# Kernel optimization log

Measured on AMD Instinct MI355X. Metric: run time of the kernel, lower is better.

Reference implementation:

```python
import jax, jax.numpy as jnp
import numpy as np

DICT_SIZE = 16384
D_MODEL = 1024
TOP_K = 8
B, T = 2, 2048


def setup_inputs() -> dict:
    key = jax.random.key(0)
    k1, k2, k3 = jax.random.split(key, 3)
    x = jax.random.normal(k1, (B, T, D_MODEL), dtype=jnp.float32)
    # nn.Linear weight, scaled small like the torch init style
    W_enc = jax.random.normal(k2, (DICT_SIZE, D_MODEL), dtype=jnp.float32) * 0.02
    # unified dictionary: randn * 0.02 per UnifiedDictionaryCore
    W_dict = jax.random.normal(k3, (DICT_SIZE, D_MODEL), dtype=jnp.float32) * 0.02
    return {"x": x, "W_enc": W_enc, "W_dict": W_dict}


def reference(x, W_enc, W_dict):
    # encoder: Linear(d_model -> dict_size), no bias
    coeffs = jnp.einsum("btd,md->btm", x, W_enc)  # [B,T,dict_size]
    topk_vals, topk_idx = jax.lax.top_k(coeffs, TOP_K)  # [B,T,K]
    # scatter-into-zeros then dense matmul == weighted sum of gathered dict rows
    # (top-k indices are unique per token, so the math is identical)
    rows = W_dict[topk_idx]  # [B,T,K,d_model]
    offset = jnp.einsum("btk,btkd->btd", topk_vals, rows)
    # sparse_coeffs.abs().mean() over the full dense [B,T,dict_size] tensor;
    # only the top-k entries are nonzero
    sparsity_loss = jnp.sum(jnp.abs(topk_vals)) / (coeffs.size)
    return offset, sparsity_loss
```

## Files before the change

kernel.cpp:

```cpp
#include <hip/hip_runtime.h>
#include <float.h>
#include <stdint.h>

constexpr int D_MODEL = 1024;
constexpr int DICT    = 16384;
constexpr int TOPK    = 8;
constexpr int NCAND   = 16;
constexpr int NTOK    = 4096;
constexpr int NTILE   = 128;
constexpr long long COEFF_COUNT = (long long)NTOK * DICT;

typedef __attribute__((ext_vector_type(8))) __bf16 bf16x8;
typedef __attribute__((ext_vector_type(4))) float  floatx4;

__device__ __forceinline__ unsigned short f2bf(float f) {
    unsigned int u = __float_as_uint(f);
    u = u + 0x7fffu + ((u >> 16) & 1u);
    return (unsigned short)(u >> 16);
}

__device__ __forceinline__ void async16(void* lds, const void* g) {
    __builtin_amdgcn_global_load_lds(
        (__attribute__((address_space(1))) void*)g,
        (__attribute__((address_space(3))) void*)lds, 16, 0, 0);
}

__global__ __launch_bounds__(256) void ssod_cvt2(const float4* __restrict__ xs, ushort4* __restrict__ xd, int nx4,
                                                 const float4* __restrict__ ws, ushort4* __restrict__ wd, int nw4) {
    const int i = blockIdx.x * 256 + threadIdx.x;
    if (i < nx4) {
        const float4 v = xs[i];
        ushort4 o; o.x = f2bf(v.x); o.y = f2bf(v.y); o.z = f2bf(v.z); o.w = f2bf(v.w);
        xd[i] = o;
    } else {
        const int j = i - nx4;
        if (j < nw4) {
            const float4 v = ws[j];
            ushort4 o; o.x = f2bf(v.x); o.y = f2bf(v.y); o.z = f2bf(v.z); o.w = f2bf(v.w);
            wd[j] = o;
        }
    }
}

constexpr size_t R1OFF = (size_t)128 * (D_MODEL * 2);

#define STAGE_A(buf_, t_) do {                                               \
    const char* s_ = pA + (size_t)(t_) * 64;                                 \
    char* d_ = (char*)&As[(buf_)][0] + wave * 1024;                          \
    async16(d_, s_); async16(d_ + 8192, s_ + R1OFF);                         \
} while (0)

#define STAGE_B(buf_, t_) do {                                               \
    const char* s_ = pB + (size_t)(t_) * 64;                                 \
    char* d_ = (char*)&Bs[(buf_)][0] + wave * 1024;                          \
    async16(d_, s_); async16(d_ + 8192, s_ + R1OFF);                         \
} while (0)

#define MFMA4(a_, r_)                                                                        \
    acc[r_][0] = __builtin_amdgcn_mfma_f32_16x16x32_bf16(a_, bq0, acc[r_][0], 0, 0, 0);      \
    acc[r_][1] = __builtin_amdgcn_mfma_f32_16x16x32_bf16(a_, bq1, acc[r_][1], 0, 0, 0);      \
    acc[r_][2] = __builtin_amdgcn_mfma_f32_16x16x32_bf16(a_, bq2, acc[r_][2], 0, 0, 0);      \
    acc[r_][3] = __builtin_amdgcn_mfma_f32_16x16x32_bf16(a_, bq3, acc[r_][3], 0, 0, 0);

#define TILE_BODY(T_, DOSTAGE_)                                              \
  {                                                                          \
    const int buf_ = (T_) & 3;                                               \
    const char* ab_ = (const char*)As + buf_ * 16384 + aob;                  \
    const char* bb_ = (const char*)Bs + buf_ * 16384 + bob;                  \
    bf16x8 af0 = *(const bf16x8*)(ab_);                                      \
    bf16x8 af1 = *(const bf16x8*)(ab_ + 1024);                               \
    bf16x8 af2 = *(const bf16x8*)(ab_ + 2048);                               \
    bf16x8 af3 = *(const bf16x8*)(ab_ + 3072);                               \
    bf16x8 bq0 = *(const bf16x8*)(bb_);                                      \
    bf16x8 bq1 = *(const bf16x8*)(bb_ + 1024);                               \
    bf16x8 bq2 = *(const bf16x8*)(bb_ + 2048);                               \
    bf16x8 bq3 = *(const bf16x8*)(bb_ + 3072);                               \
    if (DOSTAGE_) { STAGE_A(((T_) + 3) & 3, (T_) + 3); }                     \
    __builtin_amdgcn_s_barrier();                                            \
    asm volatile("s_waitcnt lgkmcnt(0)" ::: "memory");                       \
    __builtin_amdgcn_s_setprio(1);                                           \
    MFMA4(af0, 0); MFMA4(af1, 1); MFMA4(af2, 2); MFMA4(af3, 3);              \
    __builtin_amdgcn_s_setprio(0);                                           \
    __builtin_amdgcn_s_barrier();                                            \
    bf16x8 ag0 = *(const bf16x8*)(ab_ + 4096);                               \
    bf16x8 ag1 = *(const bf16x8*)(ab_ + 5120);                               \
    bf16x8 ag2 = *(const bf16x8*)(ab_ + 6144);                               \
    bf16x8 ag3 = *(const bf16x8*)(ab_ + 7168);                               \
    if (DOSTAGE_) { STAGE_B(((T_) + 3) & 3, (T_) + 3); }                     \
    __builtin_amdgcn_s_barrier();                                            \
    asm volatile("s_waitcnt lgkmcnt(0)" ::: "memory");                       \
    __builtin_amdgcn_s_setprio(1);                                           \
    MFMA4(ag0, 4); MFMA4(ag1, 5); MFMA4(ag2, 6); MFMA4(ag3, 7);              \
    __builtin_amdgcn_s_setprio(0);                                           \
  }

#define TILE_CLOSE(VMI)                                                      \
    asm volatile("s_waitcnt vmcnt(" #VMI ")" ::: "memory");                  \
    __builtin_amdgcn_s_barrier();

__global__ __launch_bounds__(512, 2) void ssod_gemm_bf16(const unsigned short* __restrict__ A,
                                                         const unsigned short* __restrict__ B,
                                                         unsigned short* __restrict__ C,
                                                         unsigned short* __restrict__ tmax,
                                                         int mtiles) {
    __shared__ __align__(16) unsigned short As[4][8192];
    __shared__ __align__(16) unsigned short Bs[4][8192];

    const int tid  = threadIdx.x;
    const int wave = tid >> 6;
    const int lane = tid & 63;

    const int nwg = mtiles * 64;
    const int cpx = nwg >> 3;
    const int bid = blockIdx.x;
    const int vid = (bid & 7) * cpx + (bid >> 3);
    const int bn  = vid & 63;
    const int bm  = vid >> 6;

    const int wm = wave >> 2;
    const int wn = wave & 3;
    const int fr = lane & 15;
    const int kg = lane >> 4;

    const int sR   = tid >> 3;
    const int sinp = ((tid & 7) * 16) ^ ((sR & 7) << 4);
    const int smr  = 2 * sR + (sinp >> 6);
    const int skb  = sinp & 63;
    const char* pA = (const char*)(A + (size_t)bm * 256 * D_MODEL) + (size_t)smr * (D_MODEL * 2) + skb;
    const char* pB = (const char*)(B + (size_t)bn * 256 * D_MODEL) + (size_t)smr * (D_MODEL * 2) + skb;

    const int swz = ((((fr & 1) << 6) | (kg << 4)) ^ (((fr >> 1) & 7) << 4));
    const int aob = (wm * 64 + (fr >> 1)) * 128 + swz;
    const int bob = (wn * 32 + (fr >> 1)) * 128 + swz;

    floatx4 acc[8][4];
    #pragma unroll
    for (int i = 0; i < 8; ++i)
        #pragma unroll
        for (int j = 0; j < 4; ++j) acc[i][j] = floatx4{0.f, 0.f, 0.f, 0.f};

    STAGE_A(0, 0); STAGE_B(0, 0);
    STAGE_A(1, 1); STAGE_B(1, 1);
    STAGE_A(2, 2); STAGE_B(2, 2);
    TILE_CLOSE(8)

    #pragma unroll 1
    for (int T = 0; T < 29; ++T) {
        TILE_BODY(T, true)
        TILE_CLOSE(8)
    }
    TILE_BODY(29, false)
    TILE_CLOSE(4)
    TILE_BODY(30, false)
    TILE_CLOSE(0)
    TILE_BODY(31, false)

    __syncthreads();
    unsigned int* rmax = (unsigned int*)&As[0][0];
    rmax[tid] = 0;
    __syncthreads();

    const int col  = lane & 15;
    const int rq   = lane >> 4;
    const int half = wn >> 1;
    const size_t colbase = (size_t)bn * 256 + wn * 64 + col;

    #pragma unroll
    for (int mf = 0; mf < 8; ++mf) {
        const int rowl = wm * 128 + mf * 16 + rq * 4;
        unsigned int rm[4] = {0, 0, 0, 0};
        #pragma unroll
        for (int nf = 0; nf < 4; ++nf) {
            unsigned short* cp = C + (size_t)(bm * 256 + rowl) * DICT + colbase + nf * 16;
            #pragma unroll
            for (int r = 0; r < 4; ++r) {
                const unsigned short bfv = f2bf(acc[mf][nf][r]);
                cp[(size_t)r * DICT] = bfv;
                rm[r] = max(rm[r], (unsigned int)(bfv ^ 0x8000u));
            }
        }
        #pragma unroll
        for (int r = 0; r < 4; ++r) {
            unsigned int m = rm[r];
            m = max(m, (unsigned int)__shfl_xor((int)m, 1, 64));
            m = max(m, (unsigned int)__shfl_xor((int)m, 2, 64));
            m = max(m, (unsigned int)__shfl_xor((int)m, 4, 64));
            m = max(m, (unsigned int)__shfl_xor((int)m, 8, 64));
            if (col == 0) atomicMax(&rmax[(rowl + r) * 2 + half], m);
        }
    }
    __syncthreads();
    {
        const int row = tid >> 1;
        tmax[(size_t)(bm * 256 + row) * NTILE + bn * 2 + (tid & 1)] = (unsigned short)rmax[tid];
    }
}

#undef TILE_BODY
#undef TILE_CLOSE
#undef MFMA4
#undef STAGE_A
#undef STAGE_B

__device__ __forceinline__ bool tk_better(float v1, int i1, float v2, int i2) {
    return (v1 > v2) || (v1 == v2 && i1 < i2);
}

__global__ __launch_bounds__(256) void ssod_select_refine(const unsigned short* __restrict__ coeffs,
                                                          const unsigned short* __restrict__ tmax,
                                                          const float* __restrict__ x,
                                                          const float* __restrict__ Wenc,
                                                          const float* __restrict__ Wdict,
                                                          float* __restrict__ outp,
                                                          float* __restrict__ tsum,
                                                          int tokBase) {
    const int tl   = blockIdx.x;
    const int t    = tokBase + tl;
    const int tid  = threadIdx.x;
    const int lane = tid & 63;
    const int wave = tid >> 6;

    __shared__ unsigned int keys[128];
    __shared__ int   tlist[64];
    __shared__ int   ncnt, kcnt;
    __shared__ unsigned int sTau;
    __shared__ float xs[D_MODEL];
    __shared__ int   cidx[NCAND];
    __shared__ float cval[NCAND];
    __shared__ float sval[TOPK];
    __shared__ int   sidx[TOPK];

    ((float4*)xs)[tid] = ((const float4*)(x + (size_t)t * D_MODEL))[tid];
    if (tid == 0) { ncnt = 0; kcnt = 0; }
    __syncthreads();

    const unsigned short* tmrow = tmax + (size_t)t * NTILE;
    if (wave == 0) {
        const unsigned int u = ((const unsigned int*)tmrow)[lane];
        unsigned int v0 = u & 0xFFFFu, v1 = u >> 16;
        for (int k = 2; k <= 128; k <<= 1) {
            for (int j = k >> 1; j >= 1; j >>= 1) {
                if (j == 64) {
                    const unsigned int a = max(v0, v1), b = min(v0, v1);
                    v0 = a; v1 = b;
                } else {
                    const unsigned int p0 = __shfl_xor(v0, j, 64);
                    const unsigned int p1 = __shfl_xor(v1, j, 64);
                    const bool tm0 = ((lane & j) == 0) ^ ((( lane      ) & k) != 0);
                    const bool tm1 = ((lane & j) == 0) ^ (((lane + 64) & k) != 0);
                    v0 = tm0 ? max(v0, p0) : min(v0, p0);
                    v1 = tm1 ? max(v1, p1) : min(v1, p1);
                }
            }
        }
        if (lane == 15) sTau = v0;
    }
    __syncthreads();
    const unsigned int tau = sTau;

    if (tid < NTILE) {
        if ((unsigned int)tmrow[tid] >= tau) {
            const int p = atomicAdd(&ncnt, 1);
            if (p < 64) tlist[p] = tid;
        }
    }
    __syncthreads();
    const int nq = min(ncnt, 64);

    const uint4* row4 = (const uint4*)(coeffs + (size_t)tl * DICT);
    for (int j = tid; j < nq * 16; j += 256) {
        const int tile = tlist[j >> 4];
        const int sub  = j & 15;
        const uint4 p = row4[tile * 16 + sub];
        unsigned int w[4] = {p.x ^ 0x80008000u, p.y ^ 0x80008000u,
                             p.z ^ 0x80008000u, p.w ^ 0x80008000u};
        const int base = tile * 128 + sub * 8;
        #pragma unroll
        for (int h = 0; h < 4; ++h) {
            const unsigned int lo = w[h] & 0xFFFFu, hi = w[h] >> 16;
            if (lo >= tau) {
                const int q = atomicAdd(&kcnt, 1);
                if (q < 128) keys[q] = (lo << 16) | (unsigned)(16383 - (base + h * 2));
            }
            if (hi >= tau) {
                const int q = atomicAdd(&kcnt, 1);
                if (q < 128) keys[q] = (hi << 16) | (unsigned)(16383 - (base + h * 2 + 1));
            }
        }
    }
    __syncthreads();
    const int m = min(kcnt, 128);
    for (int i = m + tid; i < 128; i += 256) keys[i] = 0;
    __syncthreads();

    if (wave == 0) {
        unsigned int v0 = keys[lane], v1 = keys[lane + 64];
        for (int k = 2; k <= 128; k <<= 1) {
            for (int j = k >> 1; j >= 1; j >>= 1) {
                if (j == 64) {
                    const unsigned int a = max(v0, v1), b = min(v0, v1);
                    v0 = a; v1 = b;
                } else {
                    const unsigned int p0 = __shfl_xor(v0, j, 64);
                    const unsigned int p1 = __shfl_xor(v1, j, 64);
                    const bool tm0 = ((lane & j) == 0) ^ ((( lane      ) & k) != 0);
                    const bool tm1 = ((lane & j) == 0) ^ (((lane + 64) & k) != 0);
                    v0 = tm0 ? max(v0, p0) : min(v0, p0);
                    v1 = tm1 ? max(v1, p1) : min(v1, p1);
                }
            }
        }
        if (lane < NCAND) cidx[lane] = 16383 - (int)(v0 & 0xFFFFu);
    }
    __syncthreads();

    const float4* xs4 = (const float4*)xs;
    float4 xv[4];
    #pragma unroll
    for (int q = 0; q < 4; ++q) xv[q] = xs4[q * 64 + lane];

    float4 wv[4][4];
    #pragma unroll
    for (int s = 0; s < 4; ++s) {
        const float4* wr4 = (const float4*)(Wenc + (size_t)cidx[s * 4 + wave] * D_MODEL);
        #pragma unroll
        for (int q = 0; q < 4; ++q) wv[s][q] = wr4[q * 64 + lane];
    }
    #pragma unroll
    for (int s = 0; s < 4; ++s) {
        float sum = 0.f;
        #pragma unroll
        for (int q = 0; q < 4; ++q)
            sum += xv[q].x * wv[s][q].x + xv[q].y * wv[s][q].y +
                   xv[q].z * wv[s][q].z + xv[q].w * wv[s][q].w;
        #pragma unroll
        for (int off = 32; off > 0; off >>= 1) sum += __shfl_down(sum, off, 64);
        if (lane == 0) cval[s * 4 + wave] = sum;
    }
    __syncthreads();

    if (tid < NCAND) {
        const float v = cval[tid];
        const int  ix = cidx[tid];
        int rank = 0;
        #pragma unroll
        for (int j = 0; j < NCAND; ++j)
            rank += (j != tid) && tk_better(cval[j], cidx[j], v, ix);
        if (rank < TOPK) { sval[rank] = v; sidx[rank] = ix; }
    }
    __syncthreads();
    if (tid == 0) {
        float s = 0.f;
        #pragma unroll
        for (int k = 0; k < TOPK; ++k) s += fabsf(sval[k]);
        tsum[t] = s;
    }

    const int dd = tid * 4;
    float4 a = make_float4(0.f, 0.f, 0.f, 0.f);
    #pragma unroll
    for (int k = 0; k < TOPK; ++k) {
        const float4 r = *(const float4*)(Wdict + (size_t)sidx[k] * D_MODEL + dd);
        const float s = sval[k];
        a.x += s * r.x; a.y += s * r.y; a.z += s * r.z; a.w += s * r.w;
    }
    *(float4*)(outp + (size_t)t * D_MODEL + dd) = a;
}

__global__ __launch_bounds__(256) void ssod_loss(const float* __restrict__ tsum,
                                                 float* __restrict__ out) {
    float s = 0.f;
    for (int i = threadIdx.x; i < NTOK; i += 256) s += tsum[i];
    #pragma unroll
    for (int off = 32; off > 0; off >>= 1) s += __shfl_down(s, off, 64);
    __shared__ float wsum[4];
    if ((threadIdx.x & 63) == 0) wsum[threadIdx.x >> 6] = s;
    __syncthreads();
    if (threadIdx.x == 0) {
        const float tot = wsum[0] + wsum[1] + wsum[2] + wsum[3];
        out[(size_t)NTOK * D_MODEL] = tot / (float)COEFF_COUNT;
    }
}

extern "C" void kernel_launch(void* const* d_in, const int* in_sizes, int n_in,
                              void* d_out, int out_size, void* d_ws, size_t ws_size,
                              hipStream_t stream) {
    const float* x     = (const float*)d_in[0];
    const float* Wenc  = (const float*)d_in[1];
    const float* Wdict = (const float*)d_in[2];
    float* out = (float*)d_out;

    char* ws = (char*)d_ws;
    size_t off = 0;
    unsigned short* xbf  = (unsigned short*)(ws + off); off += (size_t)NTOK * D_MODEL * 2;
    unsigned short* wbf  = (unsigned short*)(ws + off); off += (size_t)DICT * D_MODEL * 2;
    unsigned short* tmax = (unsigned short*)(ws + off); off += (size_t)NTOK * NTILE * 2;
    float* tsum = (float*)(ws + off);                   off += (size_t)NTOK * 4;
    unsigned short* coeffs = (unsigned short*)(ws + off);

    const size_t remain = (ws_size > off) ? (ws_size - off) : 0;
    int chunk = 512;
    if (remain >= (size_t)4096 * DICT * 2) chunk = 4096;
    else if (remain >= (size_t)2048 * DICT * 2) chunk = 2048;
    else if (remain >= (size_t)1024 * DICT * 2) chunk = 1024;

    const int nx4 = NTOK * D_MODEL / 4;
    const int nw4 = DICT * D_MODEL / 4;
    ssod_cvt2<<<(nx4 + nw4 + 255) / 256, 256, 0, stream>>>(
        (const float4*)x, (ushort4*)xbf, nx4, (const float4*)Wenc, (ushort4*)wbf, nw4);

    for (int tokBase = 0; tokBase < NTOK; tokBase += chunk) {
        const int mtiles = chunk / 256;
        ssod_gemm_bf16<<<mtiles * 64, 512, 0, stream>>>(xbf + (size_t)tokBase * D_MODEL, wbf, coeffs,
                                                        tmax + (size_t)tokBase * NTILE, mtiles);
        ssod_select_refine<<<chunk, 256, 0, stream>>>(coeffs, tmax, x, Wenc, Wdict, out, tsum, tokBase);
    }
    ssod_loss<<<1, 256, 0, stream>>>(tsum, out);
}
```

Baseline: 397.6 us.

## Double-buffer GEMM register fragments and swap MFMA operands for packed coefficient stores

The bf16 GEMM main loop now keeps two register sets of LDS fragments and prefetches the next tile's fragments between the two halves of the current tile's MFMAs. This replaces the old split-barrier scheme and cuts the barriers per tile from three to one. The MFMA operands are swapped so each lane holds four consecutive dictionary columns, which lets the epilogue write 8-byte packed stores instead of scalar 2-byte strided stores. The row-max reduction needs fewer shuffles as a result. The workgroup-to-tile mapping is also simplified to a fixed 8x8 swizzle, which raises register pressure at occupancy 2 and may change L2 locality.

```diff
diff --git a/kernel.cpp b/kernel.cpp
--- a/kernel.cpp
+++ b/kernel.cpp
@@ -56,53 +56,50 @@
     async16(d_, s_); async16(d_ + 8192, s_ + R1OFF);                         \
 } while (0)
 
-#define MFMA4(a_, r_)                                                                        \
-    acc[r_][0] = __builtin_amdgcn_mfma_f32_16x16x32_bf16(a_, bq0, acc[r_][0], 0, 0, 0);      \
-    acc[r_][1] = __builtin_amdgcn_mfma_f32_16x16x32_bf16(a_, bq1, acc[r_][1], 0, 0, 0);      \
-    acc[r_][2] = __builtin_amdgcn_mfma_f32_16x16x32_bf16(a_, bq2, acc[r_][2], 0, 0, 0);      \
-    acc[r_][3] = __builtin_amdgcn_mfma_f32_16x16x32_bf16(a_, bq3, acc[r_][3], 0, 0, 0);
-
-#define TILE_BODY(T_, DOSTAGE_)                                              \
-  {                                                                          \
-    const int buf_ = (T_) & 3;                                               \
-    const char* ab_ = (const char*)As + buf_ * 16384 + aob;                  \
-    const char* bb_ = (const char*)Bs + buf_ * 16384 + bob;                  \
-    bf16x8 af0 = *(const bf16x8*)(ab_);                                      \
-    bf16x8 af1 = *(const bf16x8*)(ab_ + 1024);                               \
-    bf16x8 af2 = *(const bf16x8*)(ab_ + 2048);                               \
-    bf16x8 af3 = *(const bf16x8*)(ab_ + 3072);                               \
-    bf16x8 bq0 = *(const bf16x8*)(bb_);                                      \
-    bf16x8 bq1 = *(const bf16x8*)(bb_ + 1024);                               \
-    bf16x8 bq2 = *(const bf16x8*)(bb_ + 2048);                               \
-    bf16x8 bq3 = *(const bf16x8*)(bb_ + 3072);                               \
-    if (DOSTAGE_) { STAGE_A(((T_) + 3) & 3, (T_) + 3); }                     \
-    __builtin_amdgcn_s_barrier();                                            \
-    asm volatile("s_waitcnt lgkmcnt(0)" ::: "memory");                       \
+#define LOADFRAGS(P, buf_) do {                                              \
+    const char* ab_ = (const char*)As + (buf_) * 16384 + aob;                \
+    const char* bb_ = (const char*)Bs + (buf_) * 16384 + bob;                \
+    P##af0 = *(const bf16x8*)(ab_);                                          \
+    P##af1 = *(const bf16x8*)(ab_ + 1024);                                   \
+    P##af2 = *(const bf16x8*)(ab_ + 2048);                                   \
+    P##af3 = *(const bf16x8*)(ab_ + 3072);                                   \
+    P##af4 = *(const bf16x8*)(ab_ + 4096);                                   \
+    P##af5 = *(const bf16x8*)(ab_ + 5120);                                   \
+    P##af6 = *(const bf16x8*)(ab_ + 6144);                                   \
+    P##af7 = *(const bf16x8*)(ab_ + 7168);                                   \
+    P##bq0 = *(const bf16x8*)(bb_);                                          \
+    P##bq1 = *(const bf16x8*)(bb_ + 1024);                                   \
+    P##bq2 = *(const bf16x8*)(bb_ + 2048);                                   \
+    P##bq3 = *(const bf16x8*)(bb_ + 3072);                                   \
+} while (0)
+
+#define MROW(P, AF, m_)                                                                     \
+    acc[m_][0] = __builtin_amdgcn_mfma_f32_16x16x32_bf16(P##bq0, AF, acc[m_][0], 0, 0, 0);  \
+    acc[m_][1] = __builtin_amdgcn_mfma_f32_16x16x32_bf16(P##bq1, AF, acc[m_][1], 0, 0, 0);  \
+    acc[m_][2] = __builtin_amdgcn_mfma_f32_16x16x32_bf16(P##bq2, AF, acc[m_][2], 0, 0, 0);  \
+    acc[m_][3] = __builtin_amdgcn_mfma_f32_16x16x32_bf16(P##bq3, AF, acc[m_][3], 0, 0, 0);
+
+#define C1(P) MROW(P, P##af0, 0) MROW(P, P##af1, 1) MROW(P, P##af2, 2) MROW(P, P##af3, 3)
+#define C2(P) MROW(P, P##af4, 4) MROW(P, P##af5, 5) MROW(P, P##af6, 6) MROW(P, P##af7, 7)
+
+#define TILE(T_, CONS, LOAD, DOSTAGE, VMI) do {                              \
+    if (DOSTAGE) {                                                           \
+        STAGE_A(((T_) + 3) & 3, (T_) + 3);                                   \
+        STAGE_B(((T_) + 3) & 3, (T_) + 3);                                   \
+    }                                                                        \
+    asm volatile("s_waitcnt vmcnt(" #VMI ")" ::: "memory");                  \
+    asm volatile("s_barrier" ::: "memory");                                  \
     __builtin_amdgcn_s_setprio(1);                                           \
-    MFMA4(af0, 0); MFMA4(af1, 1); MFMA4(af2, 2); MFMA4(af3, 3);              \
+    C1(CONS)                                                                 \
+    LOADFRAGS(LOAD, ((T_) + 1) & 3);                                         \
+    C2(CONS)                                                                 \
     __builtin_amdgcn_s_setprio(0);                                           \
-    __builtin_amdgcn_s_barrier();                                            \
-    bf16x8 ag0 = *(const bf16x8*)(ab_ + 4096);                               \
-    bf16x8 ag1 = *(const bf16x8*)(ab_ + 5120);                               \
-    bf16x8 ag2 = *(const bf16x8*)(ab_ + 6144);                               \
-    bf16x8 ag3 = *(const bf16x8*)(ab_ + 7168);                               \
-    if (DOSTAGE_) { STAGE_B(((T_) + 3) & 3, (T_) + 3); }                     \
-    __builtin_amdgcn_s_barrier();                                            \
-    asm volatile("s_waitcnt lgkmcnt(0)" ::: "memory");                       \
-    __builtin_amdgcn_s_setprio(1);                                           \
-    MFMA4(ag0, 4); MFMA4(ag1, 5); MFMA4(ag2, 6); MFMA4(ag3, 7);              \
-    __builtin_amdgcn_s_setprio(0);                                           \
-  }
-
-#define TILE_CLOSE(VMI)                                                      \
-    asm volatile("s_waitcnt vmcnt(" #VMI ")" ::: "memory");                  \
-    __builtin_amdgcn_s_barrier();
+} while (0)
 
 __global__ __launch_bounds__(512, 2) void ssod_gemm_bf16(const unsigned short* __restrict__ A,
                                                          const unsigned short* __restrict__ B,
                                                          unsigned short* __restrict__ C,
-                                                         unsigned short* __restrict__ tmax,
-                                                         int mtiles) {
+                                                         unsigned short* __restrict__ tmax) {
     __shared__ __align__(16) unsigned short As[4][8192];
     __shared__ __align__(16) unsigned short Bs[4][8192];
 
@@ -110,12 +107,9 @@
     const int wave = tid >> 6;
     const int lane = tid & 63;
 
-    const int nwg = mtiles * 64;
-    const int cpx = nwg >> 3;
     const int bid = blockIdx.x;
-    const int vid = (bid & 7) * cpx + (bid >> 3);
-    const int bn  = vid & 63;
-    const int bm  = vid >> 6;
+    const int bn  = (bid & 7) * 8 + ((bid >> 3) & 7);
+    const int bm  = bid >> 6;
 
     const int wm = wave >> 2;
     const int wn = wave & 3;
@@ -139,66 +133,69 @@
         #pragma unroll
         for (int j = 0; j < 4; ++j) acc[i][j] = floatx4{0.f, 0.f, 0.f, 0.f};
 
+    bf16x8 RA_af0, RA_af1, RA_af2, RA_af3, RA_af4, RA_af5, RA_af6, RA_af7;
+    bf16x8 RA_bq0, RA_bq1, RA_bq2, RA_bq3;
+    bf16x8 RB_af0, RB_af1, RB_af2, RB_af3, RB_af4, RB_af5, RB_af6, RB_af7;
+    bf16x8 RB_bq0, RB_bq1, RB_bq2, RB_bq3;
+
     STAGE_A(0, 0); STAGE_B(0, 0);
     STAGE_A(1, 1); STAGE_B(1, 1);
     STAGE_A(2, 2); STAGE_B(2, 2);
-    TILE_CLOSE(8)
+    asm volatile("s_waitcnt vmcnt(8)" ::: "memory");
+    asm volatile("s_barrier" ::: "memory");
+    LOADFRAGS(RA_, 0);
 
     #pragma unroll 1
-    for (int T = 0; T < 29; ++T) {
-        TILE_BODY(T, true)
-        TILE_CLOSE(8)
-    }
-    TILE_BODY(29, false)
-    TILE_CLOSE(4)
-    TILE_BODY(30, false)
-    TILE_CLOSE(0)
-    TILE_BODY(31, false)
+    for (int T = 0; T < 28; T += 2) {
+        TILE(T,     RA_, RB_, true, 8);
+        TILE(T + 1, RB_, RA_, true, 8);
+    }
+    TILE(28, RA_, RB_, true,  8);
+    TILE(29, RB_, RA_, false, 4);
+    TILE(30, RA_, RB_, false, 0);
+    __builtin_amdgcn_s_setprio(1);
+    C1(RB_)
+    C2(RB_)
+    __builtin_amdgcn_s_setprio(0);
 
     __syncthreads();
     unsigned int* rmax = (unsigned int*)&As[0][0];
     rmax[tid] = 0;
     __syncthreads();
 
-    const int col  = lane & 15;
-    const int rq   = lane >> 4;
-    const int half = wn >> 1;
-    const size_t colbase = (size_t)bn * 256 + wn * 64 + col;
+    const int tcol  = lane & 15;
+    const int rq4   = (lane >> 4) * 4;
+    const int half  = wn >> 1;
+    const int dbase = bn * 256 + wn * 64 + rq4;
 
     #pragma unroll
     for (int mf = 0; mf < 8; ++mf) {
-        const int rowl = wm * 128 + mf * 16 + rq * 4;
-        unsigned int rm[4] = {0, 0, 0, 0};
+        const int tok = wm * 128 + mf * 16 + tcol;
+        unsigned int tm = 0;
         #pragma unroll
         for (int nf = 0; nf < 4; ++nf) {
-            unsigned short* cp = C + (size_t)(bm * 256 + rowl) * DICT + colbase + nf * 16;
-            #pragma unroll
-            for (int r = 0; r < 4; ++r) {
-                const unsigned short bfv = f2bf(acc[mf][nf][r]);
-                cp[(size_t)r * DICT] = bfv;
-                rm[r] = max(rm[r], (unsigned int)(bfv ^ 0x8000u));
-            }
-        }
-        #pragma unroll
-        for (int r = 0; r < 4; ++r) {
-            unsigned int m = rm[r];
-            m = max(m, (unsigned int)__shfl_xor((int)m, 1, 64));
-            m = max(m, (unsigned int)__shfl_xor((int)m, 2, 64));
-            m = max(m, (unsigned int)__shfl_xor((int)m, 4, 64));
-            m = max(m, (unsigned int)__shfl_xor((int)m, 8, 64));
-            if (col == 0) atomicMax(&rmax[(rowl + r) * 2 + half], m);
-        }
-    }
-    __syncthreads();
-    {
-        const int row = tid >> 1;
-        tmax[(size_t)(bm * 256 + row) * NTILE + bn * 2 + (tid & 1)] = (unsigned short)rmax[tid];
-    }
-}
-
-#undef TILE_BODY
-#undef TILE_CLOSE
-#undef MFMA4
+            const floatx4 a = acc[mf][nf];
+            const unsigned int b0 = f2bf(a[0]), b1 = f2bf(a[1]);
+            const unsigned int b2 = f2bf(a[2]), b3 = f2bf(a[3]);
+            tm = max(tm, max(max(b0 ^ 0x8000u, b1 ^ 0x8000u),
+                             max(b2 ^ 0x8000u, b3 ^ 0x8000u)));
+            uint2 pk; pk.x = b0 | (b1 << 16); pk.y = b2 | (b3 << 16);
+            *(uint2*)(C + (size_t)(bm * 256 + tok) * DICT + dbase + nf * 16) = pk;
+        }
+        tm = max(tm, (unsigned int)__shfl_xor((int)tm, 16, 64));
+        tm = max(tm, (unsigned int)__shfl_xor((int)tm, 32, 64));
+        if (lane < 16) atomicMax(&rmax[tok * 2 + half], tm);
+    }
+    __syncthreads();
+    tmax[(size_t)(bm * 256 + (tid >> 1)) * NTILE + bn * 2 + (tid & 1)] =
+        (unsigned short)rmax[tid];
+}
+
+#undef TILE
+#undef C1
+#undef C2
+#undef MROW
+#undef LOADFRAGS
 #undef STAGE_A
 #undef STAGE_B
 
@@ -412,7 +409,7 @@
     for (int tokBase = 0; tokBase < NTOK; tokBase += chunk) {
         const int mtiles = chunk / 256;
         ssod_gemm_bf16<<<mtiles * 64, 512, 0, stream>>>(xbf + (size_t)tokBase * D_MODEL, wbf, coeffs,
-                                                        tmax + (size_t)tokBase * NTILE, mtiles);
+                                                        tmax + (size_t)tokBase * NTILE);
         ssod_select_refine<<<chunk, 256, 0, stream>>>(coeffs, tmax, x, Wenc, Wdict, out, tsum, tokBase);
     }
     ssod_loss<<<1, 256, 0, stream>>>(tsum, out);
```

Result: faster. 360.1 us (-9.4%).
